# Optimization experiments

Hardware: AMD Instinct MI355X
Metric: run time of the kernel (lower is better)

## Reference

```python
import jax, jax.numpy as jnp
import numpy as np

LN_EPS = 1e-5


def _layer_norm(x, g, b):
    m = jnp.mean(x, axis=-1, keepdims=True)
    v = jnp.mean(jnp.square(x - m), axis=-1, keepdims=True)
    return (x - m) * jax.lax.rsqrt(v + LN_EPS) * g + b


def _transition(x, g, bln, w_sw, w_ss, w_sig, b_sig, w_scale, residual):
    # TransitionBlock, eval mode (dropout = identity)
    x_in = x
    x = _layer_norm(x, g, bln)
    b = jax.nn.silu(x @ w_sw.T) * (x @ w_ss.T)
    y = jax.nn.sigmoid(x @ w_sig.T + b_sig) * (b @ w_scale.T)
    return x_in + y if residual else y


def setup_inputs() -> dict:
    N, E = 1000000, 100000
    F_DIM, A_DIM, H_DIM, HEADS = 64, 128, 256, 4
    D_IN = F_DIM + A_DIM
    key = jax.random.key(0)
    ks = jax.random.split(key, 16)
    s = 0.02
    inp = {
        'v_equivariant': jax.random.normal(ks[0], (N, 3), jnp.float32),
        'v_atom_features': jax.random.normal(ks[1], (N, A_DIM), jnp.float32),
        'edge_group_idx': jnp.sort(jax.random.randint(ks[2], (N,), 0, E)).astype(jnp.int32),
        'num_edges': E,
        'fourier_w': jax.random.normal(ks[3], (F_DIM,), jnp.float32),
        'fourier_b': jax.random.normal(ks[4], (F_DIM,), jnp.float32),
        # TransitionBlock 1 (input 192 -> 256, no residual)
        'tb1_ln_g': jnp.ones((D_IN,), jnp.float32),
        'tb1_ln_b': jnp.zeros((D_IN,), jnp.float32),
        'tb1_w_sw': jax.random.normal(ks[5], (H_DIM, D_IN), jnp.float32) * s,
        'tb1_w_ss': jax.random.normal(ks[6], (H_DIM, D_IN), jnp.float32) * s,
        'tb1_w_sig': jax.random.normal(ks[7], (H_DIM, D_IN), jnp.float32) * s,
        'tb1_b_sig': jnp.full((H_DIM,), -2.0, jnp.float32),
        'tb1_w_scale': jax.random.normal(ks[8], (H_DIM, H_DIM), jnp.float32) * s,
        # TransitionBlock 2 (256 -> 256, residual)
        'tb2_ln_g': jnp.ones((H_DIM,), jnp.float32),
        'tb2_ln_b': jnp.zeros((H_DIM,), jnp.float32),
        'tb2_w_sw': jax.random.normal(ks[9], (H_DIM, H_DIM), jnp.float32) * s,
        'tb2_w_ss': jax.random.normal(ks[10], (H_DIM, H_DIM), jnp.float32) * s,
        'tb2_w_sig': jax.random.normal(ks[11], (H_DIM, H_DIM), jnp.float32) * s,
        'tb2_b_sig': jnp.full((H_DIM,), -2.0, jnp.float32),
        'tb2_w_scale': jax.random.normal(ks[12], (H_DIM, H_DIM), jnp.float32) * s,
        # final linear 256 -> num_heads
        'out_w': jax.random.normal(ks[13], (HEADS, H_DIM), jnp.float32) * s,
        'out_b': jnp.zeros((HEADS,), jnp.float32),
    }
    return inp


def reference(v_equivariant, v_atom_features, edge_group_idx, num_edges,
              fourier_w, fourier_b,
              tb1_ln_g, tb1_ln_b, tb1_w_sw, tb1_w_ss, tb1_w_sig, tb1_b_sig, tb1_w_scale,
              tb2_ln_g, tb2_ln_b, tb2_w_sw, tb2_w_ss, tb2_w_sig, tb2_b_sig, tb2_w_scale,
              out_w, out_b):
    # Fourier embedding of vector norms: [N] -> [N, F_DIM]
    v_norms = jnp.linalg.norm(v_equivariant, axis=-1)
    f_dist = jnp.cos(2.0 * jnp.pi * (v_norms[..., None] * fourier_w + fourier_b))
    x = jnp.concatenate([f_dist, v_atom_features], axis=-1)  # [N, 192]
    x = _transition(x, tb1_ln_g, tb1_ln_b, tb1_w_sw, tb1_w_ss, tb1_w_sig, tb1_b_sig, tb1_w_scale, residual=False)
    x = _transition(x, tb2_ln_g, tb2_ln_b, tb2_w_sw, tb2_w_ss, tb2_w_sig, tb2_b_sig, tb2_w_scale, residual=True)
    scores = x @ out_w.T + out_b  # [N, H]
    # scatter_softmax over edge groups (per head)
    smax = jax.ops.segment_max(scores, edge_group_idx, num_segments=num_edges)
    e = jnp.exp(scores - smax[edge_group_idx])
    ssum = jax.ops.segment_sum(e, edge_group_idx, num_segments=num_edges)
    alphas = e / ssum[edge_group_idx]  # [N, H]
    # weighted scatter-sum pooling of 3-vectors per head
    v_weighted = v_equivariant[:, None, :] * alphas[..., None]  # [N, H, 3]
    v_pooled = jax.ops.segment_sum(v_weighted, edge_group_idx, num_segments=num_edges)
    return v_pooled.reshape(num_edges, -1)  # [E, H*3]
```

## Files before the change

### kernel.cpp

```cpp
#include <hip/hip_runtime.h>
#include <math.h>

#define DIN   192
#define HD    256
#define ROWS  32
#define THREADS 256
#define LSTR  256

typedef __bf16 bf16_t;
typedef bf16_t bf16x8 __attribute__((ext_vector_type(8)));
typedef unsigned short u16x8 __attribute__((ext_vector_type(8)));
typedef float  f32x16 __attribute__((ext_vector_type(16)));

static __device__ __forceinline__ f32x16 mfma32(bf16x8 a, bf16x8 b, f32x16 c) {
  return __builtin_amdgcn_mfma_f32_32x32x16_bf16(a, b, c, 0, 0, 0);
}
static __device__ __forceinline__ unsigned short f2bfu(float f) {
  bf16_t h = (bf16_t)f; unsigned short u; __builtin_memcpy(&u, &h, 2); return u;
}
static __device__ __forceinline__ float bfu2f(unsigned short u) {
  unsigned x = ((unsigned)u) << 16; float f; __builtin_memcpy(&f, &x, 4); return f;
}
static __device__ __forceinline__ unsigned pk2(float a, float b) {
  return (unsigned)f2bfu(a) | ((unsigned)f2bfu(b) << 16);
}
static __device__ __forceinline__ float lo16(unsigned u) { return bfu2f((unsigned short)(u & 0xffff)); }
static __device__ __forceinline__ float hi16(unsigned u) { return bfu2f((unsigned short)(u >> 16)); }
static __device__ __forceinline__ float sigm(float x) {
  return __builtin_amdgcn_rcpf(1.f + __expf(-x));
}
static __device__ __forceinline__ int lidx(int row, int col) {
  return row * LSTR + (col ^ ((row & 7) << 3));
}
static __device__ __forceinline__ int crow(int r, int kg) {
  return (r & 3) + 8 * (r >> 2) + 4 * kg;
}

#define OFF_WSW1 0
#define OFF_WSS1 49152
#define OFF_WSG1 98304
#define OFF_WSC1 147456
#define OFF_WSW2 212992
#define OFF_WSS2 278528
#define OFF_WSG2 344064
#define OFF_WSC2 409600
#define OFF_WOUT 475136
#define NGRP_REORD 59392
#define NGRP_ALL   60416

__global__ void iab_wconv_kernel(const float* __restrict__ a0, const float* __restrict__ a1,
                                 const float* __restrict__ a2, const float* __restrict__ a3,
                                 const float* __restrict__ a4, const float* __restrict__ a5,
                                 const float* __restrict__ a6, const float* __restrict__ a7,
                                 const float* __restrict__ a8, unsigned short* __restrict__ out)
{
  const int i = blockIdx.x * 256 + threadIdx.x;
  if (i >= NGRP_ALL) return;
  if (i >= NGRP_REORD) {
    const int g  = i - NGRP_REORD;
    const int ks = g >> 6;
    const int ln = g & 63;
    const int col = ln & 31;
    const int kg  = ln >> 5;
    #pragma unroll
    for (int j = 0; j < 8; ++j) {
      const float vv = (col < 4) ? a8[col * 256 + ks * 16 + kg * 8 + j] : 0.f;
      out[OFF_WOUT + (size_t)g * 8 + j] = f2bfu(vv);
    }
    return;
  }
  const float* src; int off, Kd, g;
  if      (i < 6144)  { src = a0; off = OFF_WSW1; Kd = 192; g = i; }
  else if (i < 12288) { src = a1; off = OFF_WSS1; Kd = 192; g = i - 6144; }
  else if (i < 18432) { src = a2; off = OFF_WSG1; Kd = 192; g = i - 12288; }
  else if (i < 26624) { src = a3; off = OFF_WSC1; Kd = 256; g = i - 18432; }
  else if (i < 34816) { src = a4; off = OFF_WSW2; Kd = 256; g = i - 26624; }
  else if (i < 43008) { src = a5; off = OFF_WSS2; Kd = 256; g = i - 34816; }
  else if (i < 51200) { src = a6; off = OFF_WSG2; Kd = 256; g = i - 43008; }
  else                { src = a7; off = OFF_WSC2; Kd = 256; g = i - 51200; }
  const int KS   = Kd >> 4;
  const int tile = g / (KS * 64);
  const int rem  = g - tile * (KS * 64);
  const int ks   = rem >> 6;
  const int ln   = rem & 63;
  const float* sp = src + (size_t)(tile * 32 + (ln & 31)) * Kd + ks * 16 + (ln >> 5) * 8;
  #pragma unroll
  for (int j = 0; j < 8; ++j) out[off + (size_t)g * 8 + j] = f2bfu(sp[j]);
}

template<int KS>
static __device__ __forceinline__ void gemm1(const unsigned short* __restrict__ Wt,
                                             const unsigned short* __restrict__ sIn,
                                             int l31, int kg, int xr, f32x16& acc)
{
  #pragma unroll 4
  for (int ks = 0; ks < KS; ++ks) {
    const bf16x8 Wc = *(const bf16x8*)(Wt + ks * 512);
    const bf16x8 A  = *(const bf16x8*)(sIn + l31 * LSTR + (((ks * 16) + kg * 8) ^ xr));
    acc = mfma32(A, Wc, acc);
  }
}

template<int KS>
static __device__ __forceinline__ void gemm1p(const unsigned short* __restrict__ Wa,
                                              const unsigned short* __restrict__ Wb,
                                              const unsigned short* __restrict__ sIn,
                                              int l31, int kg, int xr,
                                              f32x16& u, f32x16& s)
{
  #pragma unroll 4
  for (int ks = 0; ks < KS; ++ks) {
    const bf16x8 wa = *(const bf16x8*)(Wa + ks * 512);
    const bf16x8 wb = *(const bf16x8*)(Wb + ks * 512);
    const bf16x8 A  = *(const bf16x8*)(sIn + l31 * LSTR + (((ks * 16) + kg * 8) ^ xr));
    u = mfma32(A, wa, u);
    s = mfma32(A, wb, s);
  }
}

static __device__ __forceinline__ void storeSilu1(unsigned short* dst, const f32x16 u,
                                                  const f32x16 s, int kg, int ocol)
{
  #pragma unroll
  for (int i = 0; i < 16; ++i) {
    const float x = u[i];
    dst[lidx(crow(i, kg), ocol)] = f2bfu(x * sigm(x) * s[i]);
  }
}

static __device__ __forceinline__ void storePk1(unsigned short* dst, const unsigned* xp,
                                                int kg, int ocol)
{
  #pragma unroll
  for (int p = 0; p < 8; ++p) {
    const int row0 = crow(2 * p, kg);
    const unsigned pk = xp[p];
    dst[lidx(row0,     ocol)] = (unsigned short)(pk & 0xffff);
    dst[lidx(row0 + 1, ocol)] = (unsigned short)(pk >> 16);
  }
}

template<int KS>
static __device__ __forceinline__ void bphase(const unsigned short* __restrict__ Wa,
                                              const unsigned short* __restrict__ Wb,
                                              const unsigned short* __restrict__ sIn,
                                              unsigned short* sOut,
                                              int l31, int kg, int xr, int ocol)
{
  f32x16 u{}, s{};
  gemm1p<KS>(Wa, Wb, sIn, l31, kg, xr, u, s);
  storeSilu1(sOut, u, s, kg, ocol);
}

template<int KSG, int KSC, int RES>
static __device__ __forceinline__ void cphase(const unsigned short* __restrict__ Wg,
                                              const unsigned short* __restrict__ Wc_,
                                              const unsigned short* __restrict__ sAin,
                                              const unsigned short* __restrict__ sBin,
                                              int l31, int kg, int xr, float bias,
                                              unsigned (&xp)[8])
{
  f32x16 g{};
  gemm1<KSG>(Wg, sAin, l31, kg, xr, g);
  f32x16 c{};
  gemm1<KSC>(Wc_, sBin, l31, kg, xr, c);
  #pragma unroll
  for (int p = 0; p < 8; ++p) {
    const float y0 = sigm(g[2*p]   + bias) * c[2*p];
    const float y1 = sigm(g[2*p+1] + bias) * c[2*p+1];
    if (RES) xp[p] = pk2(lo16(xp[p]) + y0, hi16(xp[p]) + y1);
    else     xp[p] = pk2(y0, y1);
  }
}

#define LNACC(P) { \
  float e_; \
  e_ = bfu2f(P[0]); s += e_; sq += e_ * e_; \
  e_ = bfu2f(P[1]); s += e_; sq += e_ * e_; \
  e_ = bfu2f(P[2]); s += e_; sq += e_ * e_; \
  e_ = bfu2f(P[3]); s += e_; sq += e_ * e_; \
  e_ = bfu2f(P[4]); s += e_; sq += e_ * e_; \
  e_ = bfu2f(P[5]); s += e_; sq += e_ * e_; \
  e_ = bfu2f(P[6]); s += e_; sq += e_ * e_; \
  e_ = bfu2f(P[7]); s += e_; sq += e_ * e_; }

#define LNNORM(P, GPTR, BPTR, BASE) { \
  const int base_ = (BASE); \
  const float4 ga_ = *(const float4*)((GPTR) + base_); \
  const float4 gb_ = *(const float4*)((GPTR) + base_ + 4); \
  const float4 oa_ = *(const float4*)((BPTR) + base_); \
  const float4 ob_ = *(const float4*)((BPTR) + base_ + 4); \
  u16x8 q_; \
  q_[0] = f2bfu((bfu2f(P[0]) - mean) * rstd * ga_.x + oa_.x); \
  q_[1] = f2bfu((bfu2f(P[1]) - mean) * rstd * ga_.y + oa_.y); \
  q_[2] = f2bfu((bfu2f(P[2]) - mean) * rstd * ga_.z + oa_.z); \
  q_[3] = f2bfu((bfu2f(P[3]) - mean) * rstd * ga_.w + oa_.w); \
  q_[4] = f2bfu((bfu2f(P[4]) - mean) * rstd * gb_.x + ob_.x); \
  q_[5] = f2bfu((bfu2f(P[5]) - mean) * rstd * gb_.y + ob_.y); \
  q_[6] = f2bfu((bfu2f(P[6]) - mean) * rstd * gb_.z + ob_.z); \
  q_[7] = f2bfu((bfu2f(P[7]) - mean) * rstd * gb_.w + ob_.w); \
  *(u16x8*)(sA + r * LSTR + (base_ ^ xrr)) = q_; }

__global__ __launch_bounds__(THREADS, 3)
void iab_rows_mfma(
    const float* __restrict__ v, const float* __restrict__ af,
    const float* __restrict__ fw, const float* __restrict__ fb,
    const float* __restrict__ ln1g, const float* __restrict__ ln1b,
    const float* __restrict__ bsig1,
    const float* __restrict__ ln2g, const float* __restrict__ ln2b,
    const float* __restrict__ bsig2,
    const float* __restrict__ outb,
    const unsigned short* __restrict__ wc,
    float* __restrict__ scores, int N)
{
  __shared__ __align__(16) unsigned short sA[ROWS * LSTR];
  __shared__ __align__(16) unsigned short sB[ROWS * LSTR];

  const int t    = threadIdx.x;
  const int w    = t >> 6;
  const int lane = t & 63;
  const int l31  = lane & 31;
  const int kg   = lane >> 5;
  const int xr   = (lane & 7) << 3;
  const int row0 = blockIdx.x * ROWS;
  const int oc0  = w * 64 + l31;
  const int oc1  = oc0 + 32;
  const int T0   = w * 2;
  const int T1   = w * 2 + 1;
  const int lb   = lane * 8;

  {
    const int r   = t >> 3;
    const int sub = t & 7;
    const int g   = row0 + r;
    const int xrr = (r & 7) << 3;
    float s = 0.f, sq = 0.f;
    u16x8 p0, p1 = {}, p2 = {};
    {
      float vx = 0.f, vy = 0.f, vz = 0.f;
      if (g < N) {
        vx = v[3 * (size_t)g + 0];
        vy = v[3 * (size_t)g + 1];
        vz = v[3 * (size_t)g + 2];
      }
      const float nrm = sqrtf(vx * vx + vy * vy + vz * vz);
      const float4 fwa = *(const float4*)(fw + sub * 8);
      const float4 fwb = *(const float4*)(fw + sub * 8 + 4);
      const float4 fba = *(const float4*)(fb + sub * 8);
      const float4 fbb = *(const float4*)(fb + sub * 8 + 4);
      const float e0 = __cosf(6.283185307179586f * (nrm * fwa.x + fba.x));
      const float e1 = __cosf(6.283185307179586f * (nrm * fwa.y + fba.y));
      const float e2 = __cosf(6.283185307179586f * (nrm * fwa.z + fba.z));
      const float e3 = __cosf(6.283185307179586f * (nrm * fwa.w + fba.w));
      const float e4 = __cosf(6.283185307179586f * (nrm * fwb.x + fbb.x));
      const float e5 = __cosf(6.283185307179586f * (nrm * fwb.y + fbb.y));
      const float e6 = __cosf(6.283185307179586f * (nrm * fwb.z + fbb.z));
      const float e7 = __cosf(6.283185307179586f * (nrm * fwb.w + fbb.w));
      s  += e0 + e1 + e2 + e3 + e4 + e5 + e6 + e7;
      sq += e0*e0 + e1*e1 + e2*e2 + e3*e3 + e4*e4 + e5*e5 + e6*e6 + e7*e7;
      p0[0] = f2bfu(e0); p0[1] = f2bfu(e1); p0[2] = f2bfu(e2); p0[3] = f2bfu(e3);
      p0[4] = f2bfu(e4); p0[5] = f2bfu(e5); p0[6] = f2bfu(e6); p0[7] = f2bfu(e7);
    }
    if (g < N) {
      const float* ap = af + (size_t)g * 128 + sub * 8;
      {
        const float4 a0 = *(const float4*)(ap);
        const float4 a1 = *(const float4*)(ap + 4);
        s  += a0.x + a0.y + a0.z + a0.w + a1.x + a1.y + a1.z + a1.w;
        sq += a0.x*a0.x + a0.y*a0.y + a0.z*a0.z + a0.w*a0.w
            + a1.x*a1.x + a1.y*a1.y + a1.z*a1.z + a1.w*a1.w;
        p1[0] = f2bfu(a0.x); p1[1] = f2bfu(a0.y); p1[2] = f2bfu(a0.z); p1[3] = f2bfu(a0.w);
        p1[4] = f2bfu(a1.x); p1[5] = f2bfu(a1.y); p1[6] = f2bfu(a1.z); p1[7] = f2bfu(a1.w);
      }
      {
        const float4 a2 = *(const float4*)(ap + 64);
        const float4 a3 = *(const float4*)(ap + 68);
        s  += a2.x + a2.y + a2.z + a2.w + a3.x + a3.y + a3.z + a3.w;
        sq += a2.x*a2.x + a2.y*a2.y + a2.z*a2.z + a2.w*a2.w
            + a3.x*a3.x + a3.y*a3.y + a3.z*a3.z + a3.w*a3.w;
        p2[0] = f2bfu(a2.x); p2[1] = f2bfu(a2.y); p2[2] = f2bfu(a2.z); p2[3] = f2bfu(a2.w);
        p2[4] = f2bfu(a3.x); p2[5] = f2bfu(a3.y); p2[6] = f2bfu(a3.z); p2[7] = f2bfu(a3.w);
      }
    }
    #pragma unroll
    for (int o = 1; o < 8; o <<= 1) {
      s  += __shfl_xor(s,  o);
      sq += __shfl_xor(sq, o);
    }
    const float mean = s * (1.f / 192.f);
    const float var  = fmaxf(sq * (1.f / 192.f) - mean * mean, 0.f);
    const float rstd = rsqrtf(var + 1e-5f);
    LNNORM(p0, ln1g, ln1b, sub * 8);
    LNNORM(p1, ln1g, ln1b, 64 + sub * 8);
    LNNORM(p2, ln1g, ln1b, 128 + sub * 8);
  }
  __syncthreads();

  unsigned x2a[8], x2b[8];

  bphase<12>(wc + OFF_WSW1 + T0 * 12 * 512 + lb,
             wc + OFF_WSS1 + T0 * 12 * 512 + lb, sA, sB, l31, kg, xr, oc0);
  __builtin_amdgcn_sched_barrier(0);
  bphase<12>(wc + OFF_WSW1 + T1 * 12 * 512 + lb,
             wc + OFF_WSS1 + T1 * 12 * 512 + lb, sA, sB, l31, kg, xr, oc1);
  __syncthreads();

  cphase<12, 16, 0>(wc + OFF_WSG1 + T0 * 12 * 512 + lb,
                    wc + OFF_WSC1 + T0 * 16 * 512 + lb,
                    sA, sB, l31, kg, xr, bsig1[oc0], x2a);
  __builtin_amdgcn_sched_barrier(0);
  cphase<12, 16, 0>(wc + OFF_WSG1 + T1 * 12 * 512 + lb,
                    wc + OFF_WSC1 + T1 * 16 * 512 + lb,
                    sA, sB, l31, kg, xr, bsig1[oc1], x2b);
  __syncthreads();

  storePk1(sA, x2a, kg, oc0);
  storePk1(sA, x2b, kg, oc1);
  __syncthreads();

  {
    const int r   = t >> 3;
    const int sub = t & 7;
    const int xrr = (r & 7) << 3;
    const u16x8 rv0 = *(const u16x8*)(sA + r * LSTR + ((sub * 32 +  0) ^ xrr));
    const u16x8 rv1 = *(const u16x8*)(sA + r * LSTR + ((sub * 32 +  8) ^ xrr));
    const u16x8 rv2 = *(const u16x8*)(sA + r * LSTR + ((sub * 32 + 16) ^ xrr));
    const u16x8 rv3 = *(const u16x8*)(sA + r * LSTR + ((sub * 32 + 24) ^ xrr));
    float s = 0.f, sq = 0.f;
    LNACC(rv0);
    LNACC(rv1);
    LNACC(rv2);
    LNACC(rv3);
    #pragma unroll
    for (int o = 1; o < 8; o <<= 1) {
      s  += __shfl_xor(s,  o);
      sq += __shfl_xor(sq, o);
    }
    const float mean = s * (1.f / 256.f);
    const float var  = fmaxf(sq * (1.f / 256.f) - mean * mean, 0.f);
    const float rstd = rsqrtf(var + 1e-5f);
    LNNORM(rv0, ln2g, ln2b, sub * 32 +  0);
    LNNORM(rv1, ln2g, ln2b, sub * 32 +  8);
    LNNORM(rv2, ln2g, ln2b, sub * 32 + 16);
    LNNORM(rv3, ln2g, ln2b, sub * 32 + 24);
  }
  __syncthreads();

  bphase<16>(wc + OFF_WSW2 + T0 * 16 * 512 + lb,
             wc + OFF_WSS2 + T0 * 16 * 512 + lb, sA, sB, l31, kg, xr, oc0);
  __builtin_amdgcn_sched_barrier(0);
  bphase<16>(wc + OFF_WSW2 + T1 * 16 * 512 + lb,
             wc + OFF_WSS2 + T1 * 16 * 512 + lb, sA, sB, l31, kg, xr, oc1);
  __syncthreads();

  cphase<16, 16, 1>(wc + OFF_WSG2 + T0 * 16 * 512 + lb,
                    wc + OFF_WSC2 + T0 * 16 * 512 + lb,
                    sA, sB, l31, kg, xr, bsig2[oc0], x2a);
  __builtin_amdgcn_sched_barrier(0);
  cphase<16, 16, 1>(wc + OFF_WSG2 + T1 * 16 * 512 + lb,
                    wc + OFF_WSC2 + T1 * 16 * 512 + lb,
                    sA, sB, l31, kg, xr, bsig2[oc1], x2b);
  __syncthreads();

  storePk1(sA, x2a, kg, oc0);
  storePk1(sA, x2b, kg, oc1);
  __syncthreads();

  if (w == 0) {
    const unsigned short* WtF = wc + OFF_WOUT + (size_t)lane * 8;
    f32x16 c{};
    #pragma unroll 4
    for (int ks = 0; ks < 16; ++ks) {
      const bf16x8 wf = *(const bf16x8*)(WtF + ks * 512);
      const bf16x8 A  = *(const bf16x8*)(sA + l31 * LSTR + (((ks * 16) + kg * 8) ^ xr));
      c = mfma32(A, wf, c);
    }
    if (l31 < 4) {
      const float bias = outb[l31];
      #pragma unroll
      for (int i = 0; i < 16; ++i) {
        const int g = row0 + crow(i, kg);
        if (g < N) scores[(size_t)g * 4 + l31] = c[i] + bias;
      }
    }
  }
}

__device__ __forceinline__ int iab_lower_bound(const int* __restrict__ a, int n, int key)
{
  int lo = 0, hi = n;
  while (lo < hi) {
    const int mid = (lo + hi) >> 1;
    if (a[mid] < key) lo = mid + 1; else hi = mid;
  }
  return lo;
}

__global__ __launch_bounds__(256)
void iab_segpool_kernel(const float* __restrict__ scores,
                        const float* __restrict__ v,
                        const int* __restrict__ gidx,
                        float* __restrict__ out, int N, int E)
{
  const int seg  = blockIdx.x * 4 + (threadIdx.x >> 6);
  const int lane = threadIdx.x & 63;
  if (seg >= E) return;

  const int lo = iab_lower_bound(gidx, N, seg);
  const int hi = iab_lower_bound(gidx, N, seg + 1);

  const int h  = lane & 3;
  const int ro = lane >> 2;

  float m = -INFINITY;
  for (int base = lo; base < hi; base += 16) {
    const int r = base + ro;
    if (r < hi) m = fmaxf(m, scores[(size_t)r * 4 + h]);
  }
  #pragma unroll
  for (int o = 4; o < 64; o <<= 1) m = fmaxf(m, __shfl_xor(m, o));

  float ssum = 0.f, w0 = 0.f, w1 = 0.f, w2 = 0.f;
  for (int base = lo; base < hi; base += 16) {
    const int r = base + ro;
    if (r < hi) {
      const float e = expf(scores[(size_t)r * 4 + h] - m);
      ssum += e;
      w0 += e * v[3 * (size_t)r + 0];
      w1 += e * v[3 * (size_t)r + 1];
      w2 += e * v[3 * (size_t)r + 2];
    }
  }
  #pragma unroll
  for (int o = 4; o < 64; o <<= 1) {
    ssum += __shfl_xor(ssum, o);
    w0   += __shfl_xor(w0, o);
    w1   += __shfl_xor(w1, o);
    w2   += __shfl_xor(w2, o);
  }

  if (ro == 0) {
    const float inv = (hi > lo) ? (1.f / ssum) : 0.f;
    out[(size_t)seg * 12 + h * 3 + 0] = w0 * inv;
    out[(size_t)seg * 12 + h * 3 + 1] = w1 * inv;
    out[(size_t)seg * 12 + h * 3 + 2] = w2 * inv;
  }
}

extern "C" void kernel_launch(void* const* d_in, const int* in_sizes, int n_in,
                              void* d_out, int out_size, void* d_ws, size_t ws_size,
                              hipStream_t stream)
{
  const float* v     = (const float*)d_in[0];
  const float* af    = (const float*)d_in[1];
  const int*   gidx  = (const int*)  d_in[2];
  const float* fw    = (const float*)d_in[4];
  const float* fb    = (const float*)d_in[5];
  const float* ln1g  = (const float*)d_in[6];
  const float* ln1b  = (const float*)d_in[7];
  const float* wsw1  = (const float*)d_in[8];
  const float* wss1  = (const float*)d_in[9];
  const float* wsig1 = (const float*)d_in[10];
  const float* bsig1 = (const float*)d_in[11];
  const float* wsc1  = (const float*)d_in[12];
  const float* ln2g  = (const float*)d_in[13];
  const float* ln2b  = (const float*)d_in[14];
  const float* wsw2  = (const float*)d_in[15];
  const float* wss2  = (const float*)d_in[16];
  const float* wsig2 = (const float*)d_in[17];
  const float* bsig2 = (const float*)d_in[18];
  const float* wsc2  = (const float*)d_in[19];
  const float* outw  = (const float*)d_in[20];
  const float* outb  = (const float*)d_in[21];

  const int N = in_sizes[0] / 3;
  const int E = out_size / 12;

  float* scores = (float*)d_ws;
  unsigned short* wcv = (unsigned short*)((char*)d_ws + (size_t)N * 4 * sizeof(float));

  hipLaunchKernelGGL(iab_wconv_kernel, dim3((NGRP_ALL + 255) / 256), dim3(256), 0, stream,
                     wsw1, wss1, wsig1, wsc1, wsw2, wss2, wsig2, wsc2, outw, wcv);

  hipLaunchKernelGGL(iab_rows_mfma, dim3((N + ROWS - 1) / ROWS), dim3(THREADS), 0, stream,
                     v, af, fw, fb, ln1g, ln1b, bsig1, ln2g, ln2b, bsig2, outb,
                     wcv, scores, N);

  hipLaunchKernelGGL(iab_segpool_kernel, dim3((E + 3) / 4), dim3(256), 0, stream,
                     scores, v, gidx, (float*)d_out, N, E);
}
```

Before: 2.148 ms.

## Process 64 rows per block and fuse gate GEMM into first phase

Doubles the rows per block from 32 to 64, so each weight fragment loaded from global memory feeds two MFMAs (two row halves) instead of one. The sigmoid-gate GEMM moves into the same K-loop as the silu/scale GEMMs, sharing the A-operand loads, and its sigmoid results are kept packed in registers. The output projection is written straight into shared memory inside the second GEMM phase, which removes a separate store pass and a barrier. The cost is doubled shared memory and many more accumulator registers, and occupancy hint drops from 3 to 2 blocks per CU.

```diff
diff --git a/kernel.cpp b/kernel.cpp
--- a/kernel.cpp
+++ b/kernel.cpp
@@ -3,7 +3,7 @@
 
 #define DIN   192
 #define HD    256
-#define ROWS  32
+#define ROWS  64
 #define THREADS 256
 #define LSTR  256
 
@@ -89,87 +89,75 @@
 }
 
 template<int KS>
-static __device__ __forceinline__ void gemm1(const unsigned short* __restrict__ Wt,
-                                             const unsigned short* __restrict__ sIn,
-                                             int l31, int kg, int xr, f32x16& acc)
-{
+static __device__ __forceinline__ void bgphase(const unsigned short* __restrict__ Wsw,
+                                               const unsigned short* __restrict__ Wss,
+                                               const unsigned short* __restrict__ Wsg,
+                                               const unsigned short* __restrict__ sIn,
+                                               unsigned short* __restrict__ sOut,
+                                               int l31, int kg, int xr, int ocol, float bias,
+                                               unsigned (&sg0)[8], unsigned (&sg1)[8])
+{
+  f32x16 u0{}, u1{}, s0{}, s1{}, g0{}, g1{};
+  #pragma unroll 2
+  for (int ks = 0; ks < KS; ++ks) {
+    const bf16x8 wa = *(const bf16x8*)(Wsw + ks * 512);
+    const bf16x8 wb = *(const bf16x8*)(Wss + ks * 512);
+    const bf16x8 wg = *(const bf16x8*)(Wsg + ks * 512);
+    const int off = ((ks * 16) + kg * 8) ^ xr;
+    const bf16x8 A0 = *(const bf16x8*)(sIn + l31 * LSTR + off);
+    const bf16x8 A1 = *(const bf16x8*)(sIn + (32 + l31) * LSTR + off);
+    u0 = mfma32(A0, wa, u0); u1 = mfma32(A1, wa, u1);
+    s0 = mfma32(A0, wb, s0); s1 = mfma32(A1, wb, s1);
+    g0 = mfma32(A0, wg, g0); g1 = mfma32(A1, wg, g1);
+  }
+  #pragma unroll
+  for (int i = 0; i < 16; ++i) {
+    const float x0 = u0[i];
+    const float x1 = u1[i];
+    sOut[lidx(crow(i, kg),      ocol)] = f2bfu(x0 * sigm(x0) * s0[i]);
+    sOut[lidx(32 + crow(i, kg), ocol)] = f2bfu(x1 * sigm(x1) * s1[i]);
+  }
+  #pragma unroll
+  for (int p = 0; p < 8; ++p) {
+    sg0[p] = pk2(sigm(g0[2*p] + bias), sigm(g0[2*p+1] + bias));
+    sg1[p] = pk2(sigm(g1[2*p] + bias), sigm(g1[2*p+1] + bias));
+  }
+}
+
+template<int RES>
+static __device__ __forceinline__ void scphase(const unsigned short* __restrict__ Wc,
+                                               const unsigned short* __restrict__ sBin,
+                                               unsigned short* __restrict__ sAout,
+                                               int l31, int kg, int xr, int ocol,
+                                               const unsigned (&sg0)[8], const unsigned (&sg1)[8],
+                                               unsigned (&x0)[8], unsigned (&x1)[8])
+{
+  f32x16 c0{}, c1{};
   #pragma unroll 4
-  for (int ks = 0; ks < KS; ++ks) {
-    const bf16x8 Wc = *(const bf16x8*)(Wt + ks * 512);
-    const bf16x8 A  = *(const bf16x8*)(sIn + l31 * LSTR + (((ks * 16) + kg * 8) ^ xr));
-    acc = mfma32(A, Wc, acc);
-  }
-}
-
-template<int KS>
-static __device__ __forceinline__ void gemm1p(const unsigned short* __restrict__ Wa,
-                                              const unsigned short* __restrict__ Wb,
-                                              const unsigned short* __restrict__ sIn,
-                                              int l31, int kg, int xr,
-                                              f32x16& u, f32x16& s)
-{
-  #pragma unroll 4
-  for (int ks = 0; ks < KS; ++ks) {
-    const bf16x8 wa = *(const bf16x8*)(Wa + ks * 512);
-    const bf16x8 wb = *(const bf16x8*)(Wb + ks * 512);
-    const bf16x8 A  = *(const bf16x8*)(sIn + l31 * LSTR + (((ks * 16) + kg * 8) ^ xr));
-    u = mfma32(A, wa, u);
-    s = mfma32(A, wb, s);
-  }
-}
-
-static __device__ __forceinline__ void storeSilu1(unsigned short* dst, const f32x16 u,
-                                                  const f32x16 s, int kg, int ocol)
-{
-  #pragma unroll
-  for (int i = 0; i < 16; ++i) {
-    const float x = u[i];
-    dst[lidx(crow(i, kg), ocol)] = f2bfu(x * sigm(x) * s[i]);
-  }
-}
-
-static __device__ __forceinline__ void storePk1(unsigned short* dst, const unsigned* xp,
-                                                int kg, int ocol)
-{
+  for (int ks = 0; ks < 16; ++ks) {
+    const bf16x8 wv = *(const bf16x8*)(Wc + ks * 512);
+    const int off = ((ks * 16) + kg * 8) ^ xr;
+    const bf16x8 A0 = *(const bf16x8*)(sBin + l31 * LSTR + off);
+    const bf16x8 A1 = *(const bf16x8*)(sBin + (32 + l31) * LSTR + off);
+    c0 = mfma32(A0, wv, c0);
+    c1 = mfma32(A1, wv, c1);
+  }
   #pragma unroll
   for (int p = 0; p < 8; ++p) {
-    const int row0 = crow(2 * p, kg);
-    const unsigned pk = xp[p];
-    dst[lidx(row0,     ocol)] = (unsigned short)(pk & 0xffff);
-    dst[lidx(row0 + 1, ocol)] = (unsigned short)(pk >> 16);
-  }
-}
-
-template<int KS>
-static __device__ __forceinline__ void bphase(const unsigned short* __restrict__ Wa,
-                                              const unsigned short* __restrict__ Wb,
-                                              const unsigned short* __restrict__ sIn,
-                                              unsigned short* sOut,
-                                              int l31, int kg, int xr, int ocol)
-{
-  f32x16 u{}, s{};
-  gemm1p<KS>(Wa, Wb, sIn, l31, kg, xr, u, s);
-  storeSilu1(sOut, u, s, kg, ocol);
-}
-
-template<int KSG, int KSC, int RES>
-static __device__ __forceinline__ void cphase(const unsigned short* __restrict__ Wg,
-                                              const unsigned short* __restrict__ Wc_,
-                                              const unsigned short* __restrict__ sAin,
-                                              const unsigned short* __restrict__ sBin,
-                                              int l31, int kg, int xr, float bias,
-                                              unsigned (&xp)[8])
-{
-  f32x16 g{};
-  gemm1<KSG>(Wg, sAin, l31, kg, xr, g);
-  f32x16 c{};
-  gemm1<KSC>(Wc_, sBin, l31, kg, xr, c);
-  #pragma unroll
-  for (int p = 0; p < 8; ++p) {
-    const float y0 = sigm(g[2*p]   + bias) * c[2*p];
-    const float y1 = sigm(g[2*p+1] + bias) * c[2*p+1];
-    if (RES) xp[p] = pk2(lo16(xp[p]) + y0, hi16(xp[p]) + y1);
-    else     xp[p] = pk2(y0, y1);
+    const float ya0 = lo16(sg0[p]) * c0[2*p],  ya1 = hi16(sg0[p]) * c0[2*p+1];
+    const float yb0 = lo16(sg1[p]) * c1[2*p],  yb1 = hi16(sg1[p]) * c1[2*p+1];
+    if (RES) {
+      x0[p] = pk2(lo16(x0[p]) + ya0, hi16(x0[p]) + ya1);
+      x1[p] = pk2(lo16(x1[p]) + yb0, hi16(x1[p]) + yb1);
+    } else {
+      x0[p] = pk2(ya0, ya1);
+      x1[p] = pk2(yb0, yb1);
+    }
+    const int r0 = crow(2 * p, kg);
+    sAout[lidx(r0,          ocol)] = (unsigned short)(x0[p] & 0xffff);
+    sAout[lidx(r0 + 1,      ocol)] = (unsigned short)(x0[p] >> 16);
+    sAout[lidx(32 + r0,     ocol)] = (unsigned short)(x1[p] & 0xffff);
+    sAout[lidx(32 + r0 + 1, ocol)] = (unsigned short)(x1[p] >> 16);
   }
 }
 
@@ -201,7 +189,7 @@
   q_[7] = f2bfu((bfu2f(P[7]) - mean) * rstd * gb_.w + ob_.w); \
   *(u16x8*)(sA + r * LSTR + (base_ ^ xrr)) = q_; }
 
-__global__ __launch_bounds__(THREADS, 3)
+__global__ __launch_bounds__(THREADS, 2)
 void iab_rows_mfma(
     const float* __restrict__ v, const float* __restrict__ af,
     const float* __restrict__ fw, const float* __restrict__ fb,
@@ -229,8 +217,9 @@
   const int T1   = w * 2 + 1;
   const int lb   = lane * 8;
 
-  {
-    const int r   = t >> 3;
+  #pragma unroll 1
+  for (int it = 0; it < 2; ++it) {
+    const int r   = (t >> 3) + it * 32;
     const int sub = t & 7;
     const int g   = row0 + r;
     const int xrr = (r & 7) << 3;
@@ -296,30 +285,30 @@
   }
   __syncthreads();
 
-  unsigned x2a[8], x2b[8];
-
-  bphase<12>(wc + OFF_WSW1 + T0 * 12 * 512 + lb,
-             wc + OFF_WSS1 + T0 * 12 * 512 + lb, sA, sB, l31, kg, xr, oc0);
+  unsigned xT0M0[8], xT0M1[8], xT1M0[8], xT1M1[8];
+  unsigned gT0M0[8], gT0M1[8], gT1M0[8], gT1M1[8];
+
+  bgphase<12>(wc + OFF_WSW1 + T0 * 12 * 512 + lb,
+              wc + OFF_WSS1 + T0 * 12 * 512 + lb,
+              wc + OFF_WSG1 + T0 * 12 * 512 + lb,
+              sA, sB, l31, kg, xr, oc0, bsig1[oc0], gT0M0, gT0M1);
   __builtin_amdgcn_sched_barrier(0);
-  bphase<12>(wc + OFF_WSW1 + T1 * 12 * 512 + lb,
-             wc + OFF_WSS1 + T1 * 12 * 512 + lb, sA, sB, l31, kg, xr, oc1);
-  __syncthreads();
-
-  cphase<12, 16, 0>(wc + OFF_WSG1 + T0 * 12 * 512 + lb,
-                    wc + OFF_WSC1 + T0 * 16 * 512 + lb,
-                    sA, sB, l31, kg, xr, bsig1[oc0], x2a);
+  bgphase<12>(wc + OFF_WSW1 + T1 * 12 * 512 + lb,
+              wc + OFF_WSS1 + T1 * 12 * 512 + lb,
+              wc + OFF_WSG1 + T1 * 12 * 512 + lb,
+              sA, sB, l31, kg, xr, oc1, bsig1[oc1], gT1M0, gT1M1);
+  __syncthreads();
+
+  scphase<0>(wc + OFF_WSC1 + T0 * 16 * 512 + lb, sB, sA,
+             l31, kg, xr, oc0, gT0M0, gT0M1, xT0M0, xT0M1);
   __builtin_amdgcn_sched_barrier(0);
-  cphase<12, 16, 0>(wc + OFF_WSG1 + T1 * 12 * 512 + lb,
-                    wc + OFF_WSC1 + T1 * 16 * 512 + lb,
-                    sA, sB, l31, kg, xr, bsig1[oc1], x2b);
-  __syncthreads();
-
-  storePk1(sA, x2a, kg, oc0);
-  storePk1(sA, x2b, kg, oc1);
-  __syncthreads();
-
-  {
-    const int r   = t >> 3;
+  scphase<0>(wc + OFF_WSC1 + T1 * 16 * 512 + lb, sB, sA,
+             l31, kg, xr, oc1, gT1M0, gT1M1, xT1M0, xT1M1);
+  __syncthreads();
+
+  #pragma unroll 1
+  for (int it = 0; it < 2; ++it) {
+    const int r   = (t >> 3) + it * 32;
     const int sub = t & 7;
     const int xrr = (r & 7) << 3;
     const u16x8 rv0 = *(const u16x8*)(sA + r * LSTR + ((sub * 32 +  0) ^ xrr));
@@ -346,40 +335,38 @@
   }
   __syncthreads();
 
-  bphase<16>(wc + OFF_WSW2 + T0 * 16 * 512 + lb,
-             wc + OFF_WSS2 + T0 * 16 * 512 + lb, sA, sB, l31, kg, xr, oc0);
+  bgphase<16>(wc + OFF_WSW2 + T0 * 16 * 512 + lb,
+              wc + OFF_WSS2 + T0 * 16 * 512 + lb,
+              wc + OFF_WSG2 + T0 * 16 * 512 + lb,
+              sA, sB, l31, kg, xr, oc0, bsig2[oc0], gT0M0, gT0M1);
   __builtin_amdgcn_sched_barrier(0);
-  bphase<16>(wc + OFF_WSW2 + T1 * 16 * 512 + lb,
-             wc + OFF_WSS2 + T1 * 16 * 512 + lb, sA, sB, l31, kg, xr, oc1);
-  __syncthreads();
-
-  cphase<16, 16, 1>(wc + OFF_WSG2 + T0 * 16 * 512 + lb,
-                    wc + OFF_WSC2 + T0 * 16 * 512 + lb,
-                    sA, sB, l31, kg, xr, bsig2[oc0], x2a);
+  bgphase<16>(wc + OFF_WSW2 + T1 * 16 * 512 + lb,
+              wc + OFF_WSS2 + T1 * 16 * 512 + lb,
+              wc + OFF_WSG2 + T1 * 16 * 512 + lb,
+              sA, sB, l31, kg, xr, oc1, bsig2[oc1], gT1M0, gT1M1);
+  __syncthreads();
+
+  scphase<1>(wc + OFF_WSC2 + T0 * 16 * 512 + lb, sB, sA,
+             l31, kg, xr, oc0, gT0M0, gT0M1, xT0M0, xT0M1);
   __builtin_amdgcn_sched_barrier(0);
-  cphase<16, 16, 1>(wc + OFF_WSG2 + T1 * 16 * 512 + lb,
-                    wc + OFF_WSC2 + T1 * 16 * 512 + lb,
-                    sA, sB, l31, kg, xr, bsig2[oc1], x2b);
-  __syncthreads();
-
-  storePk1(sA, x2a, kg, oc0);
-  storePk1(sA, x2b, kg, oc1);
-  __syncthreads();
-
-  if (w == 0) {
+  scphase<1>(wc + OFF_WSC2 + T1 * 16 * 512 + lb, sB, sA,
+             l31, kg, xr, oc1, gT1M0, gT1M1, xT1M0, xT1M1);
+  __syncthreads();
+
+  if (w < 2) {
     const unsigned short* WtF = wc + OFF_WOUT + (size_t)lane * 8;
     f32x16 c{};
     #pragma unroll 4
     for (int ks = 0; ks < 16; ++ks) {
       const bf16x8 wf = *(const bf16x8*)(WtF + ks * 512);
-      const bf16x8 A  = *(const bf16x8*)(sA + l31 * LSTR + (((ks * 16) + kg * 8) ^ xr));
+      const bf16x8 A  = *(const bf16x8*)(sA + (w * 32 + l31) * LSTR + (((ks * 16) + kg * 8) ^ xr));
       c = mfma32(A, wf, c);
     }
     if (l31 < 4) {
       const float bias = outb[l31];
       #pragma unroll
       for (int i = 0; i < 16; ++i) {
-        const int g = row0 + crow(i, kg);
+        const int g = row0 + w * 32 + crow(i, kg);
         if (g < N) scores[(size_t)g * 4 + l31] = c[i] + bias;
       }
     }
```

Result: slower. 2.417 ms (+12.5%).
